# Performance work log

Hardware: AMD Instinct MI355X
Metric: run time of the kernel (lower is better)

Reference implementation:

```python
import jax, jax.numpy as jnp
import numpy as np

# ---- static config (mirrors AttractorCore defaults / chosen shapes) ----
B, N, D, K = 4, 1024, 128, 10          # batch, particles per batch, latent_dim, num_attractors
G = 1e-3                                # gravity_strength
DAMP = 0.95                             # damping
DT = 0.1                                # adaptive_dt initial value (held fixed; adaptive rule not in source)
ITERS = 50                              # num_iterations (fixed; early-exit break removed for jit)
EPS = 1e-6                              # gravitational softening
MAXNORM = 10.0                          # stability constraint: clip position norm
HID = 64                                # PhysicsInformedBoundary hidden_dim


def _mlp2(x, w1, b1, w2, b2):
    # Linear -> Tanh -> Linear  (potential_net / kinetic_net)
    return jnp.tanh(x @ w1 + b1) @ w2 + b2


def setup_inputs() -> dict:
    key = jax.random.key(0)
    ks = jax.random.split(key, 24)

    def lin(k, fan_in, shape):
        return jax.random.normal(k, shape, jnp.float32) / np.sqrt(fan_in)

    x = jax.random.normal(ks[0], (B, N, D), jnp.float32)
    # attractors: random directions normalized to radius 2 (latent_dim != 2 branch)
    ap = jax.random.normal(ks[1], (K, D), jnp.float32)
    ap = ap / jnp.linalg.norm(ap, axis=1, keepdims=True) * 2.0
    am = jnp.ones((K,), jnp.float32) * 0.1
    v0 = jnp.zeros((K, D), jnp.float32)  # registered velocity buffer

    return {
        "x": x,
        "attractor_positions": ap,
        "attractor_masses": am,
        "init_velocities": v0,
        # HamiltonianLayer.potential_net: D -> 2D -> 1
        "pw1": lin(ks[2], D, (D, 2 * D)), "pb1": jnp.zeros((2 * D,), jnp.float32),
        "pw2": lin(ks[3], 2 * D, (2 * D, 1)), "pb2": jnp.zeros((1,), jnp.float32),
        # HamiltonianLayer.kinetic_net: D -> 2D -> 1
        "kw1": lin(ks[4], D, (D, 2 * D)), "kb1": jnp.zeros((2 * D,), jnp.float32),
        "kw2": lin(ks[5], 2 * D, (2 * D, 1)), "kb2": jnp.zeros((1,), jnp.float32),
        # PhysicsInformedBoundary: 2D -> 64 -> 64 -> D
        "bw1": lin(ks[6], 2 * D, (2 * D, HID)), "bb1": jnp.zeros((HID,), jnp.float32),
        "bw2": lin(ks[7], HID, (HID, HID)), "bb2": jnp.zeros((HID,), jnp.float32),
        "bw3": lin(ks[8], HID, (HID, D)), "bb3": jnp.zeros((D,), jnp.float32),
        # field_projection: (3D+4) -> D
        "fw": lin(ks[9], 3 * D + 4, (3 * D + 4, D)), "fb": jnp.zeros((D,), jnp.float32),
    }


def reference(x, attractor_positions, attractor_masses, init_velocities,
              pw1, pb1, pw2, pb2, kw1, kb1, kw2, kb2,
              bw1, bb1, bw2, bb2, bw3, bb3, fw, fb):
    B_, N_, D_ = x.shape
    K_ = attractor_positions.shape[0]

    parts = x.reshape(-1, D_)                                        # [B*N, D]
    masses = jnp.concatenate([jnp.full((B_ * N_,), 0.1, x.dtype),
                              jnp.tile(attractor_masses, B_)])       # [M]
    r0 = jnp.concatenate([parts, jnp.tile(attractor_positions, (B_, 1))], 0)  # [M, D]
    v0 = jnp.concatenate([jnp.zeros_like(parts), jnp.tile(init_velocities, (B_, 1))], 0)
    M = r0.shape[0]
    diag = jnp.eye(M, dtype=bool)

    def pot_sum(p):
        return _mlp2(p, pw1, pb1, pw2, pb2).sum()

    def kin_sum(q):
        return _mlp2(q, kw1, kb1, kw2, kb2).sum()

    @jax.checkpoint
    def step(carry, i):
        r, v = carry
        # all-pairs gravitational acceleration: a_i = G * sum_j m_j (r_j - r_i)/|r_ij|^3
        sq = jnp.sum(r * r, -1)
        d2 = jnp.maximum(sq[:, None] + sq[None, :] - 2.0 * (r @ r.T), EPS)
        inv3 = jnp.where(diag, 0.0, d2 ** -1.5)                      # [M, M]
        w = inv3 * masses[None, :]
        a = G * (w @ r - jnp.sum(w, 1, keepdims=True) * r)
        v = v + a * DT
        r = r + v * DT
        # PINN boundary correction: p + 0.1*tanh(net([p, v]))
        c = jnp.concatenate([r, v], -1)
        h = jnp.tanh(jnp.tanh(c @ bw1 + bb1) @ bw2 + bb2)
        r = r + 0.1 * jnp.tanh(h @ bw3 + bb3)
        # Hamiltonian Euler step every 5 iterations
        do = (i % 5) == 0
        dp = -jax.grad(pot_sum)(r)
        dq = jax.grad(kin_sum)(v)
        r = jnp.where(do, r + 0.01 * dp, r)
        v = jnp.where(do, v + 0.01 * dq, v)
        # damping + stability clip (norm <= MAXNORM)
        v = v * DAMP
        nrm = jnp.linalg.norm(r, axis=-1, keepdims=True)
        r = r * jnp.minimum(1.0, MAXNORM / jnp.maximum(nrm, 1e-12))
        return (r, v), None

    (r, v), _ = jax.lax.scan(step, (r0, v0), jnp.arange(ITERS))

    fp = r[:B_ * N_].reshape(B_, N_, D_)                             # final particles
    fa = r[B_ * N_:].reshape(B_, K_, D_)                             # final attractors

    # ---- compute_attractor_field ----
    pm = jnp.ones((B_, N_), x.dtype)
    am = jnp.broadcast_to(attractor_masses[None, :], (B_, K_))
    allm = jnp.concatenate([pm, am], 1)                              # [B, N+K]
    allp = jnp.concatenate([fp, fa], 1)                              # [B, N+K, D]
    tot = allm.sum(1, keepdims=True)
    com = (allm[..., None] * allp).sum(1) / tot                      # center of mass [B, D]
    centered = allp - com[:, None, :]
    var = (centered ** 2).mean(1)
    skew = (centered ** 3).mean(1)
    # torch.pdist over batch element 0
    p0 = allp[0]
    sq0 = jnp.sum(p0 * p0, -1)
    dmat = jnp.sqrt(jnp.maximum(sq0[:, None] + sq0[None, :] - 2.0 * p0 @ p0.T, 0.0))
    iu, ju = jnp.triu_indices(p0.shape[0], 1)
    dd = dmat[iu, ju]
    stats = jnp.stack([dd.mean(), dd.std(ddof=1), dd.min(), dd.max()])
    stats = jnp.broadcast_to(stats[None, :], (B_, 4))
    feat = jnp.concatenate([com, var, skew, stats], -1)              # [B, 3D+4]
    return feat @ fw + fb                                            # field_projection -> [B, D]


if __name__ == "__main__":
    out = reference(**setup_inputs())
    print(out.shape)
```

## Files before the change

kernel.cpp:

```cpp
#include <hip/hip_runtime.h>
#include <hip/hip_bf16.h>
#include <math.h>

#define DIM    128
#define NPART  4096
#define MREAL  4136
#define MP     4224
#define IB     64
#define NIBR   65
#define JTILE  32
#define NJTR   130
#define NSLICE 8
#define NROW   4136
#define NITER  50
#define NPTS   1034
#define NPAIRS 534061.0
#define WR     16
#define NMLPB  259

typedef __bf16 bf16x8 __attribute__((ext_vector_type(8)));
typedef float  f32x4  __attribute__((ext_vector_type(4)));

__device__ __forceinline__ f32x4 mfma16(bf16x8 a, bf16x8 b, f32x4 c) {
  return __builtin_amdgcn_mfma_f32_16x16x32_bf16(a, b, c, 0, 0, 0);
}
__device__ __forceinline__ float dot4acc(float s, float4 a, float4 b) {
  s = fmaf(a.x, b.x, s); s = fmaf(a.y, b.y, s);
  s = fmaf(a.z, b.z, s); s = fmaf(a.w, b.w, s);
  return s;
}
__device__ __forceinline__ void split3(float x, __bf16& h, __bf16& m, __bf16& l) {
  h = (__bf16)x; float t = x - (float)h;
  m = (__bf16)t; l = (__bf16)(t - (float)m);
}
__device__ __forceinline__ f32x4 mm6(bf16x8 ah, bf16x8 am, bf16x8 al,
                                     bf16x8 bh, bf16x8 bm, bf16x8 bl, f32x4 c) {
  c = mfma16(ah, bh, c);
  c = mfma16(ah, bm, c);
  c = mfma16(am, bh, c);
  c = mfma16(am, bm, c);
  c = mfma16(ah, bl, c);
  c = mfma16(al, bh, c);
  return c;
}
__device__ __forceinline__ f32x4 mm4(bf16x8 ah, bf16x8 am,
                                     bf16x8 bh, bf16x8 bm, f32x4 c) {
  c = mfma16(ah, bh, c);
  c = mfma16(ah, bm, c);
  c = mfma16(am, bh, c);
  c = mfma16(am, bm, c);
  return c;
}
__device__ __forceinline__ int lds_off(int row, int slot) {
  return row * DIM + ((slot ^ ((row >> 2) & 7)) << 2);
}
__device__ __forceinline__ int jmap(int s) {
  return 4 * (s >> 3) + (s & 3) + 16 * ((s >> 2) & 1);
}

__global__ __launch_bounds__(256)
void k_init(const float* __restrict__ x, const float* __restrict__ ap,
            const float* __restrict__ am, const float* __restrict__ v0in,
            float* __restrict__ r, float* __restrict__ v, float* __restrict__ sq)
{
  int wid = threadIdx.x >> 6, ln = threadIdx.x & 63;
  int row = blockIdx.x * 4 + wid;
  int d0 = ln, d1 = ln + 64;
  size_t base = (size_t)row * DIM;
  float r0, r1, w0, w1;
  if (row < NPART) {
    r0 = x[base + d0]; r1 = x[base + d1]; w0 = 0.f; w1 = 0.f;
  } else if (row < MREAL) {
    int k = (row - NPART) % 10;
    r0 = ap[k * DIM + d0]; r1 = ap[k * DIM + d1];
    w0 = v0in[k * DIM + d0]; w1 = v0in[k * DIM + d1];
  } else {
    r0 = r1 = w0 = w1 = 0.f;
  }
  r[base + d0] = r0; r[base + d1] = r1;
  v[base + d0] = w0; v[base + d1] = w1;
  float n2 = r0 * r0 + r1 * r1;
  for (int mk = 1; mk < 64; mk <<= 1) n2 += __shfl_xor(n2, mk);
  if (ln == 0) { sq[row] = n2; }
}

__global__ __launch_bounds__(256)
void k_wprep(const float* __restrict__ bw1, const float* __restrict__ bw2,
             const float* __restrict__ bw3, const float* __restrict__ pw1,
             const float* __restrict__ kw1,
             __bf16* __restrict__ wb1t, __bf16* __restrict__ wb2t,
             __bf16* __restrict__ wb3t, __bf16* __restrict__ wp1t,
             __bf16* __restrict__ wp1r, __bf16* __restrict__ wk1t,
             __bf16* __restrict__ wk1r)
{
  int a = blockIdx.y;
  int e = blockIdx.x * 256 + threadIdx.x;
  float val; __bf16* dst; int size;
  if (a == 0)      { size = 16384; if (e >= size) return; int n = e >> 8, k = e & 255; val = bw1[k * 64 + n];  dst = wb1t; }
  else if (a == 1) { size = 4096;  if (e >= size) return; int n = e >> 6, k = e & 63;  val = bw2[k * 64 + n];  dst = wb2t; }
  else if (a == 2) { size = 8192;  if (e >= size) return; int n = e >> 6, k = e & 63;  val = bw3[k * 128 + n]; dst = wb3t; }
  else if (a == 3) { size = 32768; if (e >= size) return; int n = e >> 7, d = e & 127; val = pw1[d * 256 + n]; dst = wp1t; }
  else if (a == 4) { size = 32768; if (e >= size) return; val = pw1[e]; dst = wp1r; }
  else if (a == 5) { size = 32768; if (e >= size) return; int n = e >> 7, d = e & 127; val = kw1[d * 256 + n]; dst = wk1t; }
  else             { size = 32768; if (e >= size) return; val = kw1[e]; dst = wk1r; }
  __bf16 h, m, l; split3(val, h, m, l);
  dst[e] = h; dst[size + e] = m; dst[2 * size + e] = l;
}

__global__ __launch_bounds__(256)
void k_split(const float* __restrict__ r,
             __bf16* __restrict__ rh, __bf16* __restrict__ rm,
             __bf16* __restrict__ rth, __bf16* __restrict__ rtm, __bf16* __restrict__ rtl)
{
  __shared__ __bf16 hs[32][132], ms2[32][132], ls[32][132];
  const int tid = threadIdx.x;
  const int row = tid >> 3, cg = tid & 7;
  const int grow = blockIdx.x * 32 + row;
  const float* rp = &r[(size_t)grow * DIM + cg * 16];
  float4 f0 = *(const float4*)&rp[0];
  float4 f1 = *(const float4*)&rp[4];
  float4 f2 = *(const float4*)&rp[8];
  float4 f3 = *(const float4*)&rp[12];
  float xs[16] = {f0.x,f0.y,f0.z,f0.w, f1.x,f1.y,f1.z,f1.w,
                  f2.x,f2.y,f2.z,f2.w, f3.x,f3.y,f3.z,f3.w};
  bf16x8 hq[2], mq[2];
  #pragma unroll
  for (int e = 0; e < 16; ++e) {
    float xv = xs[e];
    __bf16 hh, mm, ll; split3(xv, hh, mm, ll);
    hq[e >> 3][e & 7] = hh; mq[e >> 3][e & 7] = mm;
    hs[row][cg * 16 + e] = hh; ms2[row][cg * 16 + e] = mm; ls[row][cg * 16 + e] = ll;
  }
  size_t ob = (size_t)grow * DIM + cg * 16;
  *(bf16x8*)&rh[ob] = hq[0]; *(bf16x8*)&rh[ob + 8] = hq[1];
  *(bf16x8*)&rm[ob] = mq[0]; *(bf16x8*)&rm[ob + 8] = mq[1];
  __syncthreads();
  for (int u = tid; u < 384; u += 256) {
    int s = u >> 7, d = u & 127;
    const __bf16* src = s == 0 ? &hs[0][0] : (s == 1 ? &ms2[0][0] : &ls[0][0]);
    __bf16 col[32];
    #pragma unroll
    for (int j = 0; j < 32; ++j) col[j] = src[j * 132 + d];
    __bf16* dst = (s == 0 ? rth : (s == 1 ? rtm : rtl)) + (size_t)d * MP + blockIdx.x * 32;
    #pragma unroll
    for (int c = 0; c < 4; ++c) {
      bf16x8 q;
      #pragma unroll
      for (int e = 0; e < 8; ++e) q[e] = col[jmap(c * 8 + e)];
      *(bf16x8*)&dst[c * 8] = q;
    }
  }
}

__global__ __launch_bounds__(256, 3)
void k_force(const __bf16* __restrict__ rh, const __bf16* __restrict__ rm,
             const __bf16* __restrict__ rth, const __bf16* __restrict__ rtm,
             const __bf16* __restrict__ rtl,
             const float* __restrict__ sq, const float* __restrict__ am,
             float* __restrict__ apart, float* __restrict__ wsump)
{
  __shared__ __align__(16) __bf16 rjRM[2][JTILE][136];
  __shared__ __align__(16) __bf16 rjT[3][DIM][40];
  __shared__ float sqi_s[IB], sqj_s[JTILE], mj_s[JTILE];

  const int tid = threadIdx.x;
  const int wv = tid >> 6, lane = tid & 63;
  const int lq = lane >> 4, lr = lane & 15;
  const int slice = blockIdx.x;
  const int bi0 = blockIdx.y * IB;

  if (tid < IB) sqi_s[tid] = sq[bi0 + tid];

  const int u1 = tid + 256;
  const int sr0 = tid >> 4, sc0 = tid & 15;
  const int sr1 = u1 >> 4,  sc1 = u1 & 15;
  const int td0 = tid >> 2, te0 = tid & 3;
  const int td1 = u1 >> 2,  te1 = u1 & 3;

  bf16x8 pr[10];
  float psqj = 0.f, pmj = 0.f;

  auto LOADT = [&](int jt) {
    size_t ga0 = (size_t)(jt * JTILE + sr0) * DIM + sc0 * 8;
    size_t ga1 = (size_t)(jt * JTILE + sr1) * DIM + sc1 * 8;
    pr[0] = *(const bf16x8*)&rh[ga0];  pr[1] = *(const bf16x8*)&rm[ga0];
    pr[2] = *(const bf16x8*)&rh[ga1];  pr[3] = *(const bf16x8*)&rm[ga1];
    size_t gb0 = (size_t)td0 * MP + jt * JTILE + te0 * 8;
    size_t gb1 = (size_t)td1 * MP + jt * JTILE + te1 * 8;
    pr[4] = *(const bf16x8*)&rth[gb0]; pr[5] = *(const bf16x8*)&rtm[gb0];
    pr[6] = *(const bf16x8*)&rtl[gb0]; pr[7] = *(const bf16x8*)&rth[gb1];
    pr[8] = *(const bf16x8*)&rtm[gb1]; pr[9] = *(const bf16x8*)&rtl[gb1];
    if (tid < JTILE) {
      int gj = jt * JTILE + tid;
      psqj = sq[gj];
      pmj = gj < NPART ? 0.1f : (gj < MREAL ? am[(gj - NPART) % 10] : 0.f);
    }
  };
  auto STORET = [&]() {
    *(bf16x8*)&rjRM[0][sr0][sc0 * 8] = pr[0];
    *(bf16x8*)&rjRM[1][sr0][sc0 * 8] = pr[1];
    *(bf16x8*)&rjRM[0][sr1][sc1 * 8] = pr[2];
    *(bf16x8*)&rjRM[1][sr1][sc1 * 8] = pr[3];
    *(bf16x8*)&rjT[0][td0][te0 * 8] = pr[4];
    *(bf16x8*)&rjT[1][td0][te0 * 8] = pr[5];
    *(bf16x8*)&rjT[2][td0][te0 * 8] = pr[6];
    *(bf16x8*)&rjT[0][td1][te1 * 8] = pr[7];
    *(bf16x8*)&rjT[1][td1][te1 * 8] = pr[8];
    *(bf16x8*)&rjT[2][td1][te1 * 8] = pr[9];
    if (tid < JTILE) { sqj_s[tid] = psqj; mj_s[tid] = pmj; }
  };

  bf16x8 riH[4], riM[4];
  {
    int gi = bi0 + wv * 16 + lr;
    const __bf16* ph = &rh[(size_t)gi * DIM];
    const __bf16* pm = &rm[(size_t)gi * DIM];
    #pragma unroll
    for (int kc = 0; kc < 4; ++kc) {
      riH[kc] = *(const bf16x8*)&ph[kc * 32 + lq * 8];
      riM[kc] = *(const bf16x8*)&pm[kc * 32 + lq * 8];
    }
  }

  f32x4 accPV[8];
  #pragma unroll
  for (int nt = 0; nt < 8; ++nt) { f32x4 z = {0.f,0.f,0.f,0.f}; accPV[nt] = z; }
  float wsacc = 0.f;

  LOADT(slice);
  STORET();
  __syncthreads();

  for (int jt = slice; jt < NJTR; jt += NSLICE) {
    const int jn = jt + NSLICE;
    const bool more = jn < NJTR;
    if (more) LOADT(jn);

    f32x4 accST[2];
    { f32x4 z = {0.f,0.f,0.f,0.f}; accST[0] = z; accST[1] = z; }
    __builtin_amdgcn_s_setprio(1);
    #pragma unroll
    for (int kc = 0; kc < 4; ++kc) {
      int kq = kc * 4 + lq;
      #pragma unroll
      for (int nt = 0; nt < 2; ++nt) {
        int j = nt * 16 + lr;
        bf16x8 ah = *(const bf16x8*)&rjRM[0][j][kq * 8];
        bf16x8 am = *(const bf16x8*)&rjRM[1][j][kq * 8];
        accST[nt] = mm4(ah, am, riH[kc], riM[kc], accST[nt]);
      }
    }
    __builtin_amdgcn_s_setprio(0);

    bf16x8 aH, aM, aL;
    {
      const int giL = bi0 + wv * 16 + lr;
      const float sqi_l = sqi_s[wv * 16 + lr];
      #pragma unroll
      for (int nt = 0; nt < 2; ++nt)
        #pragma unroll
        for (int rr = 0; rr < 4; ++rr) {
          int jl = nt * 16 + 4 * lq + rr;
          int gj = jt * JTILE + jl;
          float d2 = fmaxf(sqi_l + sqj_s[jl] - 2.f * accST[nt][rr], 1e-6f);
          float rin = rsqrtf(d2);
          float wgt = mj_s[jl] * rin * rin * rin;
          if (giL == gj) wgt = 0.f;
          wsacc += wgt;
          __bf16 wh, wm2, wl2; split3(wgt, wh, wm2, wl2);
          int e = nt * 4 + rr;
          aH[e] = wh; aM[e] = wm2; aL[e] = wl2;
        }
    }

    {
      __builtin_amdgcn_s_setprio(1);
      #pragma unroll
      for (int nt = 0; nt < 8; ++nt) {
        int d = nt * 16 + lr;
        bf16x8 bh = *(const bf16x8*)&rjT[0][d][lq * 8];
        bf16x8 bm = *(const bf16x8*)&rjT[1][d][lq * 8];
        bf16x8 bl = *(const bf16x8*)&rjT[2][d][lq * 8];
        accPV[nt] = mm6(aH, aM, aL, bh, bm, bl, accPV[nt]);
      }
      __builtin_amdgcn_s_setprio(0);
    }

    __syncthreads();
    if (more) STORET();
    __syncthreads();
  }

  {
    float val = wsacc;
    val += __shfl_xor(val, 16);
    val += __shfl_xor(val, 32);
    int gi = bi0 + wv * 16 + lr;
    if (lane < 16 && gi < NROW) wsump[(size_t)slice * NROW + gi] = val;
  }
  #pragma unroll
  for (int nt = 0; nt < 8; ++nt)
    #pragma unroll
    for (int rr = 0; rr < 4; ++rr) {
      int gi = bi0 + wv * 16 + 4 * lq + rr;
      int d = nt * 16 + lr;
      if (gi < NROW) apart[((size_t)slice * NROW + gi) * DIM + d] = accPV[nt][rr];
    }
}

__global__ __launch_bounds__(256)
void k_mlp(float* __restrict__ r, float* __restrict__ v, float* __restrict__ sq,
           const float* __restrict__ apart, const float* __restrict__ wsump,
           const __bf16* __restrict__ wb1t, const __bf16* __restrict__ wb2t,
           const __bf16* __restrict__ wb3t,
           const __bf16* __restrict__ wp1t, const __bf16* __restrict__ wp1r,
           const __bf16* __restrict__ wk1t, const __bf16* __restrict__ wk1r,
           const float* __restrict__ bb1, const float* __restrict__ bb2,
           const float* __restrict__ bb3,
           const float* __restrict__ pb1, const float* __restrict__ pw2,
           const float* __restrict__ kb1, const float* __restrict__ kw2,
           int do_ham)
{
  __shared__ __align__(16) float  Cf[WR][264];
  __shared__ __align__(16) __bf16 Csp[3][WR][264];
  __shared__ __align__(16) __bf16 Hsp[2][3][WR][72];
  __shared__ __align__(16) __bf16 Gsp[3][WR][264];

  const int tid = threadIdx.x;
  const int wv = tid >> 6, lane = tid & 63;
  const int lq = lane >> 4, lr = lane & 15;

  {
    const int row = tid >> 4, c = tid & 15;
    const int grow = blockIdx.x * WR + row;
    const int gsrc = grow < NROW ? grow : 0;
    float s[8] = {0.f,0.f,0.f,0.f,0.f,0.f,0.f,0.f};
    float wsv = 0.f;
    #pragma unroll
    for (int sl = 0; sl < NSLICE; ++sl) {
      const float4* ap4 = (const float4*)&apart[((size_t)sl * NROW + gsrc) * DIM + c * 8];
      float4 t0 = ap4[0], t1 = ap4[1];
      s[0] += t0.x; s[1] += t0.y; s[2] += t0.z; s[3] += t0.w;
      s[4] += t1.x; s[5] += t1.y; s[6] += t1.z; s[7] += t1.w;
      wsv += wsump[(size_t)sl * NROW + gsrc];
    }
    const float4* r4 = (const float4*)&r[(size_t)gsrc * DIM + c * 8];
    const float4* v4 = (const float4*)&v[(size_t)gsrc * DIM + c * 8];
    float4 ra = r4[0], rb = r4[1], va = v4[0], vb = v4[1];
    float re[8] = {ra.x,ra.y,ra.z,ra.w, rb.x,rb.y,rb.z,rb.w};
    float ve[8] = {va.x,va.y,va.z,va.w, vb.x,vb.y,vb.z,vb.w};
    bf16x8 rh8, rm8, rl8, vh8, vm8, vl8;
    #pragma unroll
    for (int e = 0; e < 8; ++e) {
      float a = 1e-3f * (s[e] - wsv * re[e]);
      float vn = ve[e] + 0.1f * a;
      float rn = re[e] + 0.1f * vn;
      Cf[row][c * 8 + e] = rn;
      Cf[row][128 + c * 8 + e] = vn;
      __bf16 h, m, l;
      split3(rn, h, m, l); rh8[e] = h; rm8[e] = m; rl8[e] = l;
      split3(vn, h, m, l); vh8[e] = h; vm8[e] = m; vl8[e] = l;
    }
    *(bf16x8*)&Csp[0][row][c * 8] = rh8; *(bf16x8*)&Csp[0][row][128 + c * 8] = vh8;
    *(bf16x8*)&Csp[1][row][c * 8] = rm8; *(bf16x8*)&Csp[1][row][128 + c * 8] = vm8;
    *(bf16x8*)&Csp[2][row][c * 8] = rl8; *(bf16x8*)&Csp[2][row][128 + c * 8] = vl8;
  }
  __syncthreads();

  {
    f32x4 acc = {0.f, 0.f, 0.f, 0.f};
    const __bf16* b = wb1t + ((size_t)(wv * 16 + lr)) * 256;
    #pragma unroll
    for (int kc = 0; kc < 8; ++kc) {
      int k0 = kc * 32 + lq * 8;
      bf16x8 ah = *(const bf16x8*)&Csp[0][lr][k0];
      bf16x8 am = *(const bf16x8*)&Csp[1][lr][k0];
      bf16x8 al = *(const bf16x8*)&Csp[2][lr][k0];
      bf16x8 b0 = *(const bf16x8*)&b[k0];
      bf16x8 b1 = *(const bf16x8*)&b[16384 + k0];
      bf16x8 b2 = *(const bf16x8*)&b[32768 + k0];
      acc = mm6(ah, am, al, b0, b1, b2, acc);
    }
    int n = wv * 16 + lr;
    float bias = bb1[n];
    #pragma unroll
    for (int reg = 0; reg < 4; ++reg) {
      int i = 4 * lq + reg;
      float h1 = tanhf(acc[reg] + bias);
      __bf16 h, m, l; split3(h1, h, m, l);
      Hsp[0][0][i][n] = h; Hsp[0][1][i][n] = m; Hsp[0][2][i][n] = l;
    }
  }
  __syncthreads();

  {
    f32x4 acc = {0.f, 0.f, 0.f, 0.f};
    const __bf16* b = wb2t + ((size_t)(wv * 16 + lr)) * 64;
    #pragma unroll
    for (int kc = 0; kc < 2; ++kc) {
      int k0 = kc * 32 + lq * 8;
      bf16x8 ah = *(const bf16x8*)&Hsp[0][0][lr][k0];
      bf16x8 am = *(const bf16x8*)&Hsp[0][1][lr][k0];
      bf16x8 al = *(const bf16x8*)&Hsp[0][2][lr][k0];
      bf16x8 b0 = *(const bf16x8*)&b[k0];
      bf16x8 b1 = *(const bf16x8*)&b[4096 + k0];
      bf16x8 b2 = *(const bf16x8*)&b[8192 + k0];
      acc = mm6(ah, am, al, b0, b1, b2, acc);
    }
    int n = wv * 16 + lr;
    float bias = bb2[n];
    #pragma unroll
    for (int reg = 0; reg < 4; ++reg) {
      int i = 4 * lq + reg;
      float h2 = tanhf(acc[reg] + bias);
      __bf16 h, m, l; split3(h2, h, m, l);
      Hsp[1][0][i][n] = h; Hsp[1][1][i][n] = m; Hsp[1][2][i][n] = l;
    }
  }
  __syncthreads();

  {
    f32x4 acc[2];
    { f32x4 z = {0.f,0.f,0.f,0.f}; acc[0] = z; acc[1] = z; }
    #pragma unroll
    for (int kc = 0; kc < 2; ++kc) {
      int k0 = kc * 32 + lq * 8;
      bf16x8 ah = *(const bf16x8*)&Hsp[1][0][lr][k0];
      bf16x8 am = *(const bf16x8*)&Hsp[1][1][lr][k0];
      bf16x8 al = *(const bf16x8*)&Hsp[1][2][lr][k0];
      #pragma unroll
      for (int t = 0; t < 2; ++t) {
        const __bf16* b = wb3t + ((size_t)(t * 64 + wv * 16 + lr)) * 64;
        bf16x8 b0 = *(const bf16x8*)&b[k0];
        bf16x8 b1 = *(const bf16x8*)&b[8192 + k0];
        bf16x8 b2 = *(const bf16x8*)&b[16384 + k0];
        acc[t] = mm6(ah, am, al, b0, b1, b2, acc[t]);
      }
    }
    #pragma unroll
    for (int t = 0; t < 2; ++t) {
      int n = t * 64 + wv * 16 + lr;
      float bias = bb3[n];
      #pragma unroll
      for (int reg = 0; reg < 4; ++reg) {
        int i = 4 * lq + reg;
        float o = tanhf(acc[t][reg] + bias);
        float rn = Cf[i][n] + 0.1f * o;
        Cf[i][n] = rn;
        __bf16 h, m, l; split3(rn, h, m, l);
        Csp[0][i][n] = h; Csp[1][i][n] = m; Csp[2][i][n] = l;
      }
    }
  }
  __syncthreads();

  if (do_ham) {
    {
      f32x4 acc[4];
      #pragma unroll
      for (int t = 0; t < 4; ++t) { f32x4 z = {0.f,0.f,0.f,0.f}; acc[t] = z; }
      #pragma unroll
      for (int kc = 0; kc < 4; ++kc) {
        int k0 = kc * 32 + lq * 8;
        bf16x8 ah = *(const bf16x8*)&Csp[0][lr][k0];
        bf16x8 am = *(const bf16x8*)&Csp[1][lr][k0];
        bf16x8 al = *(const bf16x8*)&Csp[2][lr][k0];
        #pragma unroll
        for (int t = 0; t < 4; ++t) {
          const __bf16* b = wp1t + ((size_t)(t * 64 + wv * 16 + lr)) * 128;
          bf16x8 b0 = *(const bf16x8*)&b[k0];
          bf16x8 b1 = *(const bf16x8*)&b[32768 + k0];
          bf16x8 b2 = *(const bf16x8*)&b[65536 + k0];
          acc[t] = mm6(ah, am, al, b0, b1, b2, acc[t]);
        }
      }
      #pragma unroll
      for (int t = 0; t < 4; ++t) {
        int n = t * 64 + wv * 16 + lr;
        float pb = pb1[n], pws = pw2[n];
        #pragma unroll
        for (int reg = 0; reg < 4; ++reg) {
          int i = 4 * lq + reg;
          float tt = tanhf(acc[t][reg] + pb);
          float g = (1.f - tt * tt) * pws;
          __bf16 h, m, l; split3(g, h, m, l);
          Gsp[0][i][n] = h; Gsp[1][i][n] = m; Gsp[2][i][n] = l;
        }
      }
    }
    __syncthreads();
    {
      f32x4 acc[2];
      { f32x4 z = {0.f,0.f,0.f,0.f}; acc[0] = z; acc[1] = z; }
      #pragma unroll
      for (int kc = 0; kc < 8; ++kc) {
        int k0 = kc * 32 + lq * 8;
        bf16x8 ah = *(const bf16x8*)&Gsp[0][lr][k0];
        bf16x8 am = *(const bf16x8*)&Gsp[1][lr][k0];
        bf16x8 al = *(const bf16x8*)&Gsp[2][lr][k0];
        #pragma unroll
        for (int t = 0; t < 2; ++t) {
          const __bf16* b = wp1r + ((size_t)(t * 64 + wv * 16 + lr)) * 256;
          bf16x8 b0 = *(const bf16x8*)&b[k0];
          bf16x8 b1 = *(const bf16x8*)&b[32768 + k0];
          bf16x8 b2 = *(const bf16x8*)&b[65536 + k0];
          acc[t] = mm6(ah, am, al, b0, b1, b2, acc[t]);
        }
      }
      #pragma unroll
      for (int t = 0; t < 2; ++t)
        #pragma unroll
        for (int reg = 0; reg < 4; ++reg) {
          int i = 4 * lq + reg, d = t * 64 + wv * 16 + lr;
          float rn = Cf[i][d] - 0.01f * acc[t][reg];
          Cf[i][d] = rn;
          __bf16 h, m, l; split3(rn, h, m, l);
          Csp[0][i][d] = h; Csp[1][i][d] = m; Csp[2][i][d] = l;
        }
    }
    __syncthreads();
    {
      f32x4 acc[4];
      #pragma unroll
      for (int t = 0; t < 4; ++t) { f32x4 z = {0.f,0.f,0.f,0.f}; acc[t] = z; }
      #pragma unroll
      for (int kc = 0; kc < 4; ++kc) {
        int k0 = 128 + kc * 32 + lq * 8;
        bf16x8 ah = *(const bf16x8*)&Csp[0][lr][k0];
        bf16x8 am = *(const bf16x8*)&Csp[1][lr][k0];
        bf16x8 al = *(const bf16x8*)&Csp[2][lr][k0];
        #pragma unroll
        for (int t = 0; t < 4; ++t) {
          const __bf16* b = wk1t + ((size_t)(t * 64 + wv * 16 + lr)) * 128;
          int kb = kc * 32 + lq * 8;
          bf16x8 b0 = *(const bf16x8*)&b[kb];
          bf16x8 b1 = *(const bf16x8*)&b[32768 + kb];
          bf16x8 b2 = *(const bf16x8*)&b[65536 + kb];
          acc[t] = mm6(ah, am, al, b0, b1, b2, acc[t]);
        }
      }
      #pragma unroll
      for (int t = 0; t < 4; ++t) {
        int n = t * 64 + wv * 16 + lr;
        float kb = kb1[n], kws = kw2[n];
        #pragma unroll
        for (int reg = 0; reg < 4; ++reg) {
          int i = 4 * lq + reg;
          float tt = tanhf(acc[t][reg] + kb);
          float g = (1.f - tt * tt) * kws;
          __bf16 h, m, l; split3(g, h, m, l);
          Gsp[0][i][n] = h; Gsp[1][i][n] = m; Gsp[2][i][n] = l;
        }
      }
    }
    __syncthreads();
    {
      f32x4 acc[2];
      { f32x4 z = {0.f,0.f,0.f,0.f}; acc[0] = z; acc[1] = z; }
      #pragma unroll
      for (int kc = 0; kc < 8; ++kc) {
        int k0 = kc * 32 + lq * 8;
        bf16x8 ah = *(const bf16x8*)&Gsp[0][lr][k0];
        bf16x8 am = *(const bf16x8*)&Gsp[1][lr][k0];
        bf16x8 al = *(const bf16x8*)&Gsp[2][lr][k0];
        #pragma unroll
        for (int t = 0; t < 2; ++t) {
          const __bf16* b = wk1r + ((size_t)(t * 64 + wv * 16 + lr)) * 256;
          bf16x8 b0 = *(const bf16x8*)&b[k0];
          bf16x8 b1 = *(const bf16x8*)&b[32768 + k0];
          bf16x8 b2 = *(const bf16x8*)&b[65536 + k0];
          acc[t] = mm6(ah, am, al, b0, b1, b2, acc[t]);
        }
      }
      #pragma unroll
      for (int t = 0; t < 2; ++t)
        #pragma unroll
        for (int reg = 0; reg < 4; ++reg) {
          int i = 4 * lq + reg, d = t * 64 + wv * 16 + lr;
          Cf[i][128 + d] += 0.01f * acc[t][reg];
        }
    }
    __syncthreads();
  }

  {
    const int row = tid >> 4, c = tid & 15;
    const int grow = blockIdx.x * WR + row;
    float re[8], ve[8];
    #pragma unroll
    for (int e = 0; e < 8; ++e) {
      re[e] = Cf[row][c * 8 + e];
      ve[e] = Cf[row][128 + c * 8 + e] * 0.95f;
    }
    float n2 = 0.f;
    #pragma unroll
    for (int e = 0; e < 8; ++e) n2 += re[e] * re[e];
    n2 += __shfl_xor(n2, 1); n2 += __shfl_xor(n2, 2);
    n2 += __shfl_xor(n2, 4); n2 += __shfl_xor(n2, 8);
    float nrm = sqrtf(n2);
    float sc = fminf(1.f, 10.f / fmaxf(nrm, 1e-12f));
    if (grow < NROW) {
      float4 o0, o1, w0, w1;
      o0.x = re[0] * sc; o0.y = re[1] * sc; o0.z = re[2] * sc; o0.w = re[3] * sc;
      o1.x = re[4] * sc; o1.y = re[5] * sc; o1.z = re[6] * sc; o1.w = re[7] * sc;
      w0.x = ve[0]; w0.y = ve[1]; w0.z = ve[2]; w0.w = ve[3];
      w1.x = ve[4]; w1.y = ve[5]; w1.z = ve[6]; w1.w = ve[7];
      *(float4*)&r[(size_t)grow * DIM + c * 8] = o0;
      *(float4*)&r[(size_t)grow * DIM + c * 8 + 4] = o1;
      *(float4*)&v[(size_t)grow * DIM + c * 8] = w0;
      *(float4*)&v[(size_t)grow * DIM + c * 8 + 4] = w1;
      if (c == 0) sq[grow] = n2 * sc * sc;
    }
  }
}

__global__ void k_statinit(double* pd_sum, double* pd_sumsq,
                           unsigned* pd_min, unsigned* pd_max)
{
  if (threadIdx.x == 0) {
    *pd_sum = 0.0; *pd_sumsq = 0.0;
    *pd_min = 0x7f7fffffu;
    *pd_max = 0u;
  }
}

__global__ __launch_bounds__(256)
void k_com(const float* __restrict__ r, const float* __restrict__ am,
           float* __restrict__ feat)
{
  int b = blockIdx.x, ch = blockIdx.y;
  int c = threadIdx.x & 31, rg = threadIdx.x >> 5;
  int col = ch * 32 + c;
  __shared__ float red[8][33];
  float amsum = 0.f;
  for (int k = 0; k < 10; ++k) amsum += am[k];
  float tot = 1024.f + amsum;

  float s = 0.f;
  #pragma unroll 4
  for (int p = rg; p < NPTS; p += 8) {
    int row = p < 1024 ? b * 1024 + p : NPART + b * 10 + (p - 1024);
    float m = p < 1024 ? 1.f : am[p - 1024];
    s += m * r[(size_t)row * DIM + col];
  }
  red[rg][c] = s; __syncthreads();
  for (int h = 4; h >= 1; h >>= 1) { if (rg < h) red[rg][c] += red[rg + h][c]; __syncthreads(); }
  float com = red[0][c] / tot;
  __syncthreads();

  float s2 = 0.f, s3 = 0.f;
  #pragma unroll 4
  for (int p = rg; p < NPTS; p += 8) {
    int row = p < 1024 ? b * 1024 + p : NPART + b * 10 + (p - 1024);
    float cc = r[(size_t)row * DIM + col] - com;
    s2 += cc * cc; s3 += cc * cc * cc;
  }
  red[rg][c] = s2; __syncthreads();
  for (int h = 4; h >= 1; h >>= 1) { if (rg < h) red[rg][c] += red[rg + h][c]; __syncthreads(); }
  float var = red[0][c] / 1034.f;
  __syncthreads();
  red[rg][c] = s3; __syncthreads();
  for (int h = 4; h >= 1; h >>= 1) { if (rg < h) red[rg][c] += red[rg + h][c]; __syncthreads(); }
  float skw = red[0][c] / 1034.f;
  if (rg == 0) {
    feat[b * 384 + col]       = com;
    feat[b * 384 + 128 + col] = var;
    feat[b * 384 + 256 + col] = skw;
  }
}

__global__ __launch_bounds__(256)
void k_pdist(const float* __restrict__ r, const float* __restrict__ sq,
             double* pd_sum, double* pd_sumsq, unsigned* pd_min, unsigned* pd_max)
{
  int ta = blockIdx.x, tb = blockIdx.y;
  if (ta > tb) return;
  __shared__ __align__(16) float pa_s[64 * DIM];
  __shared__ __align__(16) float pb_s[64 * DIM];
  __shared__ float sqa_s[64], sqb_s[64];
  const int tid = threadIdx.x;
  const int tx = tid & 15, ty = tid >> 4;

  #pragma unroll
  for (int p = 0; p < 8; ++p) {
    int q = tid + p * 256;
    int row = q >> 5, slot = q & 31;
    int pidx = ta * 64 + row;
    float4 val = make_float4(0.f, 0.f, 0.f, 0.f);
    if (pidx < NPTS) {
      int srow = pidx < 1024 ? pidx : (NPART + pidx - 1024);
      val = *(const float4*)&r[(size_t)srow * DIM + slot * 4];
    }
    *(float4*)&pa_s[lds_off(row, slot)] = val;
    pidx = tb * 64 + row;
    val = make_float4(0.f, 0.f, 0.f, 0.f);
    if (pidx < NPTS) {
      int srow = pidx < 1024 ? pidx : (NPART + pidx - 1024);
      val = *(const float4*)&r[(size_t)srow * DIM + slot * 4];
    }
    *(float4*)&pb_s[lds_off(row, slot)] = val;
  }
  if (tid < 64) {
    int pidx = ta * 64 + tid;
    sqa_s[tid] = pidx < NPTS ? sq[pidx < 1024 ? pidx : NPART + pidx - 1024] : 0.f;
  } else if (tid < 128) {
    int t2 = tid - 64;
    int pidx = tb * 64 + t2;
    sqb_s[t2] = pidx < NPTS ? sq[pidx < 1024 ? pidx : NPART + pidx - 1024] : 0.f;
  }
  __syncthreads();

  const int swi = ty & 7, swj = tx & 7;
  float sv[4][4] = {};
  #pragma unroll 8
  for (int ks = 0; ks < 32; ++ks) {
    int oi = (ks ^ swi) << 2, oj = (ks ^ swj) << 2;
    float4 av[4], bv[4];
    #pragma unroll
    for (int a = 0; a < 4; ++a) av[a] = *(const float4*)&pa_s[(ty * 4 + a) * DIM + oi];
    #pragma unroll
    for (int b = 0; b < 4; ++b) bv[b] = *(const float4*)&pb_s[(tx * 4 + b) * DIM + oj];
    #pragma unroll
    for (int a = 0; a < 4; ++a)
      #pragma unroll
      for (int b = 0; b < 4; ++b) sv[a][b] = dot4acc(sv[a][b], av[a], bv[b]);
  }

  double tsum = 0.0, tsq = 0.0;
  float tmn = 3.402823466e38f, tmx = 0.f;
  #pragma unroll
  for (int a = 0; a < 4; ++a)
    #pragma unroll
    for (int b = 0; b < 4; ++b) {
      int ga = ta * 64 + ty * 4 + a;
      int gb = tb * 64 + tx * 4 + b;
      float d2 = sqa_s[ty * 4 + a] + sqb_s[tx * 4 + b] - 2.f * sv[a][b];
      float dist = sqrtf(fmaxf(d2, 0.f));
      bool ok = (ga < NPTS) && (gb < NPTS) && ((ta != tb) || (ga < gb));
      if (ok) {
        tsum += (double)dist;
        tsq  += (double)dist * (double)dist;
        tmn = fminf(tmn, dist);
        tmx = fmaxf(tmx, dist);
      }
    }
  for (int mk = 1; mk < 64; mk <<= 1) {
    tsum += __shfl_xor(tsum, mk);
    tsq  += __shfl_xor(tsq, mk);
    tmn = fminf(tmn, __shfl_xor(tmn, mk));
    tmx = fmaxf(tmx, __shfl_xor(tmx, mk));
  }
  if ((tid & 63) == 0) {
    atomicAdd(pd_sum, tsum);
    atomicAdd(pd_sumsq, tsq);
    atomicMin(pd_min, __float_as_uint(tmn));
    atomicMax(pd_max, __float_as_uint(tmx));
  }
}

__global__ void k_proj(const float* __restrict__ feat,
                       const double* pd_sum, const double* pd_sumsq,
                       const unsigned* pd_min, const unsigned* pd_max,
                       const float* __restrict__ fw, const float* __restrict__ fb,
                       float* __restrict__ out)
{
  int t = threadIdx.x;
  int b = t >> 7, d = t & 127;
  double sm = *pd_sum, s2 = *pd_sumsq;
  double mean = sm / NPAIRS;
  double var = (s2 - sm * sm / NPAIRS) / (NPAIRS - 1.0);
  float sd = (float)sqrt(var > 0.0 ? var : 0.0);
  float mn = __uint_as_float(*pd_min);
  float mx = __uint_as_float(*pd_max);
  float acc0 = fb[d], acc1 = 0.f, acc2 = 0.f, acc3 = 0.f;
  #pragma unroll 8
  for (int f = 0; f < 384; f += 4) {
    acc0 = fmaf(feat[b * 384 + f + 0], fw[(f + 0) * 128 + d], acc0);
    acc1 = fmaf(feat[b * 384 + f + 1], fw[(f + 1) * 128 + d], acc1);
    acc2 = fmaf(feat[b * 384 + f + 2], fw[(f + 2) * 128 + d], acc2);
    acc3 = fmaf(feat[b * 384 + f + 3], fw[(f + 3) * 128 + d], acc3);
  }
  float acc = (acc0 + acc1) + (acc2 + acc3);
  acc = fmaf((float)mean, fw[384 * 128 + d], acc);
  acc = fmaf(sd,          fw[385 * 128 + d], acc);
  acc = fmaf(mn,          fw[386 * 128 + d], acc);
  acc = fmaf(mx,          fw[387 * 128 + d], acc);
  out[b * 128 + d] = acc;
}

extern "C" void kernel_launch(void* const* d_in, const int* in_sizes, int n_in,
                              void* d_out, int out_size, void* d_ws, size_t ws_size,
                              hipStream_t stream) {
  (void)in_sizes; (void)n_in; (void)out_size; (void)ws_size;
  const float* x   = (const float*)d_in[0];
  const float* ap  = (const float*)d_in[1];
  const float* am  = (const float*)d_in[2];
  const float* v0  = (const float*)d_in[3];
  const float* pw1 = (const float*)d_in[4];
  const float* pb1 = (const float*)d_in[5];
  const float* pw2 = (const float*)d_in[6];
  const float* kw1 = (const float*)d_in[8];
  const float* kb1 = (const float*)d_in[9];
  const float* kw2 = (const float*)d_in[10];
  const float* bw1 = (const float*)d_in[12];
  const float* bb1 = (const float*)d_in[13];
  const float* bw2 = (const float*)d_in[14];
  const float* bb2 = (const float*)d_in[15];
  const float* bw3 = (const float*)d_in[16];
  const float* bb3 = (const float*)d_in[17];
  const float* fw  = (const float*)d_in[18];
  const float* fb  = (const float*)d_in[19];

  char* ws = (char*)d_ws;
  double*   pd_sum   = (double*)(ws + 0);
  double*   pd_sumsq = (double*)(ws + 8);
  unsigned* pd_min   = (unsigned*)(ws + 16);
  unsigned* pd_max   = (unsigned*)(ws + 20);
  float*    feat     = (float*)(ws + 32);
  float*    r        = (float*)(ws + 6176);
  float*    v        = (float*)(ws + 2168864);
  float*    sq       = (float*)(ws + 4331552);
  float*    wsump    = (float*)(ws + 4348448);
  float*    apart    = (float*)(ws + 4480800);
  __bf16*   rh       = (__bf16*)(ws + 21421856);
  __bf16*   rm       = (__bf16*)(ws + 22503200);
  __bf16*   rth      = (__bf16*)(ws + 24665888);
  __bf16*   rtm      = (__bf16*)(ws + 25747232);
  __bf16*   rtl      = (__bf16*)(ws + 26828576);
  __bf16*   wb1t     = (__bf16*)(ws + 27909920);
  __bf16*   wb2t     = (__bf16*)(ws + 28008224);
  __bf16*   wb3t     = (__bf16*)(ws + 28032800);
  __bf16*   wp1t     = (__bf16*)(ws + 28081952);
  __bf16*   wp1r     = (__bf16*)(ws + 28278560);
  __bf16*   wk1t     = (__bf16*)(ws + 28475168);
  __bf16*   wk1r     = (__bf16*)(ws + 28671776);

  k_wprep<<<dim3(128, 7), 256, 0, stream>>>(bw1, bw2, bw3, pw1, kw1,
                                            wb1t, wb2t, wb3t, wp1t, wp1r, wk1t, wk1r);
  k_init<<<MP / 4, 256, 0, stream>>>(x, ap, am, v0, r, v, sq);
  for (int it = 0; it < NITER; ++it) {
    k_split<<<NJTR, 256, 0, stream>>>(r, rh, rm, rth, rtm, rtl);
    k_force<<<dim3(NSLICE, NIBR), 256, 0, stream>>>(rh, rm, rth, rtm, rtl,
                                                    sq, am, apart, wsump);
    k_mlp<<<NMLPB, 256, 0, stream>>>(r, v, sq, apart, wsump,
        wb1t, wb2t, wb3t, wp1t, wp1r, wk1t, wk1r,
        bb1, bb2, bb3, pb1, pw2, kb1, kw2,
        (it % 5) == 0 ? 1 : 0);
  }
  k_statinit<<<1, 64, 0, stream>>>(pd_sum, pd_sumsq, pd_min, pd_max);
  k_com<<<dim3(4, 4), 256, 0, stream>>>(r, am, feat);
  k_pdist<<<dim3(17, 17), 256, 0, stream>>>(r, sq, pd_sum, pd_sumsq, pd_min, pd_max);
  k_proj<<<1, 512, 0, stream>>>(feat, pd_sum, pd_sumsq, pd_min, pd_max, fw, fb,
                                (float*)d_out);
}
```

Measured before the change: 5.267 ms.

## Fuse bf16 split into MLP epilogue and double i-tile per force block

The per-iteration k_split launch is removed. Its work now happens in the k_mlp epilogue, which writes the hi/mid/lo bf16 splits and the transposed tiles straight from shared memory, and k_split runs once before the loop. k_force now handles 128 rows per block (two 16-row m-tiles per wave), so each loaded j-tile feeds twice as many MFMAs. The next-tile prefetch is moved after the weight computation. The trade is more registers and fewer blocks (occupancy hint drops from 3 to 2 blocks per SM, and half as many i-blocks), plus extra shared-memory and global-store work in k_mlp. The transposed-write indexing in k_mlp relies on the jmap permutation pattern, so a mismatch with k_split's layout is a correctness risk.

```diff
diff --git a/kernel.cpp b/kernel.cpp
--- a/kernel.cpp
+++ b/kernel.cpp
@@ -6,8 +6,8 @@
 #define NPART  4096
 #define MREAL  4136
 #define MP     4224
-#define IB     64
-#define NIBR   65
+#define IB     128
+#define NIBT   33
 #define JTILE  32
 #define NJTR   130
 #define NSLICE 8
@@ -19,6 +19,7 @@
 #define NMLPB  259
 
 typedef __bf16 bf16x8 __attribute__((ext_vector_type(8)));
+typedef __bf16 bf16x4 __attribute__((ext_vector_type(4)));
 typedef float  f32x4  __attribute__((ext_vector_type(4)));
 
 __device__ __forceinline__ f32x4 mfma16(bf16x8 a, bf16x8 b, f32x4 c) {
@@ -152,7 +153,7 @@
   }
 }
 
-__global__ __launch_bounds__(256, 3)
+__global__ __launch_bounds__(256, 2)
 void k_force(const __bf16* __restrict__ rh, const __bf16* __restrict__ rm,
              const __bf16* __restrict__ rth, const __bf16* __restrict__ rtm,
              const __bf16* __restrict__ rtl,
@@ -210,22 +211,25 @@
     if (tid < JTILE) { sqj_s[tid] = psqj; mj_s[tid] = pmj; }
   };
 
-  bf16x8 riH[4], riM[4];
-  {
-    int gi = bi0 + wv * 16 + lr;
+  bf16x8 riH[2][4], riM[2][4];
+  #pragma unroll
+  for (int mt = 0; mt < 2; ++mt) {
+    int gi = bi0 + wv * 32 + mt * 16 + lr;
     const __bf16* ph = &rh[(size_t)gi * DIM];
     const __bf16* pm = &rm[(size_t)gi * DIM];
     #pragma unroll
     for (int kc = 0; kc < 4; ++kc) {
-      riH[kc] = *(const bf16x8*)&ph[kc * 32 + lq * 8];
-      riM[kc] = *(const bf16x8*)&pm[kc * 32 + lq * 8];
-    }
-  }
-
-  f32x4 accPV[8];
+      riH[mt][kc] = *(const bf16x8*)&ph[kc * 32 + lq * 8];
+      riM[mt][kc] = *(const bf16x8*)&pm[kc * 32 + lq * 8];
+    }
+  }
+
+  f32x4 accPV[2][8];
   #pragma unroll
-  for (int nt = 0; nt < 8; ++nt) { f32x4 z = {0.f,0.f,0.f,0.f}; accPV[nt] = z; }
-  float wsacc = 0.f;
+  for (int mt = 0; mt < 2; ++mt)
+    #pragma unroll
+    for (int nt = 0; nt < 8; ++nt) { f32x4 z = {0.f,0.f,0.f,0.f}; accPV[mt][nt] = z; }
+  float wsacc[2] = {0.f, 0.f};
 
   LOADT(slice);
   STORET();
@@ -234,10 +238,10 @@
   for (int jt = slice; jt < NJTR; jt += NSLICE) {
     const int jn = jt + NSLICE;
     const bool more = jn < NJTR;
-    if (more) LOADT(jn);
-
-    f32x4 accST[2];
-    { f32x4 z = {0.f,0.f,0.f,0.f}; accST[0] = z; accST[1] = z; }
+
+    f32x4 accST[2][2];
+    { f32x4 z = {0.f,0.f,0.f,0.f};
+      accST[0][0] = z; accST[0][1] = z; accST[1][0] = z; accST[1][1] = z; }
     __builtin_amdgcn_s_setprio(1);
     #pragma unroll
     for (int kc = 0; kc < 4; ++kc) {
@@ -246,32 +250,37 @@
       for (int nt = 0; nt < 2; ++nt) {
         int j = nt * 16 + lr;
         bf16x8 ah = *(const bf16x8*)&rjRM[0][j][kq * 8];
-        bf16x8 am = *(const bf16x8*)&rjRM[1][j][kq * 8];
-        accST[nt] = mm4(ah, am, riH[kc], riM[kc], accST[nt]);
+        bf16x8 am2 = *(const bf16x8*)&rjRM[1][j][kq * 8];
+        accST[0][nt] = mm4(ah, am2, riH[0][kc], riM[0][kc], accST[0][nt]);
+        accST[1][nt] = mm4(ah, am2, riH[1][kc], riM[1][kc], accST[1][nt]);
       }
     }
     __builtin_amdgcn_s_setprio(0);
 
-    bf16x8 aH, aM, aL;
-    {
-      const int giL = bi0 + wv * 16 + lr;
-      const float sqi_l = sqi_s[wv * 16 + lr];
+    bf16x8 aH[2], aM[2], aL[2];
+    #pragma unroll
+    for (int mt = 0; mt < 2; ++mt) {
+      const int il = wv * 32 + mt * 16 + lr;
+      const int giL = bi0 + il;
+      const float sqi_l = sqi_s[il];
       #pragma unroll
       for (int nt = 0; nt < 2; ++nt)
         #pragma unroll
         for (int rr = 0; rr < 4; ++rr) {
           int jl = nt * 16 + 4 * lq + rr;
           int gj = jt * JTILE + jl;
-          float d2 = fmaxf(sqi_l + sqj_s[jl] - 2.f * accST[nt][rr], 1e-6f);
+          float d2 = fmaxf(sqi_l + sqj_s[jl] - 2.f * accST[mt][nt][rr], 1e-6f);
           float rin = rsqrtf(d2);
           float wgt = mj_s[jl] * rin * rin * rin;
           if (giL == gj) wgt = 0.f;
-          wsacc += wgt;
+          wsacc[mt] += wgt;
           __bf16 wh, wm2, wl2; split3(wgt, wh, wm2, wl2);
           int e = nt * 4 + rr;
-          aH[e] = wh; aM[e] = wm2; aL[e] = wl2;
+          aH[mt][e] = wh; aM[mt][e] = wm2; aL[mt][e] = wl2;
         }
     }
+
+    if (more) LOADT(jn);
 
     {
       __builtin_amdgcn_s_setprio(1);
@@ -281,7 +290,8 @@
         bf16x8 bh = *(const bf16x8*)&rjT[0][d][lq * 8];
         bf16x8 bm = *(const bf16x8*)&rjT[1][d][lq * 8];
         bf16x8 bl = *(const bf16x8*)&rjT[2][d][lq * 8];
-        accPV[nt] = mm6(aH, aM, aL, bh, bm, bl, accPV[nt]);
+        accPV[0][nt] = mm6(aH[0], aM[0], aL[0], bh, bm, bl, accPV[0][nt]);
+        accPV[1][nt] = mm6(aH[1], aM[1], aL[1], bh, bm, bl, accPV[1][nt]);
       }
       __builtin_amdgcn_s_setprio(0);
     }
@@ -291,21 +301,24 @@
     __syncthreads();
   }
 
-  {
-    float val = wsacc;
+  #pragma unroll
+  for (int mt = 0; mt < 2; ++mt) {
+    float val = wsacc[mt];
     val += __shfl_xor(val, 16);
     val += __shfl_xor(val, 32);
-    int gi = bi0 + wv * 16 + lr;
+    int gi = bi0 + wv * 32 + mt * 16 + lr;
     if (lane < 16 && gi < NROW) wsump[(size_t)slice * NROW + gi] = val;
   }
   #pragma unroll
-  for (int nt = 0; nt < 8; ++nt)
-    #pragma unroll
-    for (int rr = 0; rr < 4; ++rr) {
-      int gi = bi0 + wv * 16 + 4 * lq + rr;
-      int d = nt * 16 + lr;
-      if (gi < NROW) apart[((size_t)slice * NROW + gi) * DIM + d] = accPV[nt][rr];
-    }
+  for (int mt = 0; mt < 2; ++mt)
+    #pragma unroll
+    for (int nt = 0; nt < 8; ++nt)
+      #pragma unroll
+      for (int rr = 0; rr < 4; ++rr) {
+        int gi = bi0 + wv * 32 + mt * 16 + 4 * lq + rr;
+        int d = nt * 16 + lr;
+        if (gi < NROW) apart[((size_t)slice * NROW + gi) * DIM + d] = accPV[mt][nt][rr];
+      }
 }
 
 __global__ __launch_bounds__(256)
@@ -319,6 +332,9 @@
            const float* __restrict__ bb3,
            const float* __restrict__ pb1, const float* __restrict__ pw2,
            const float* __restrict__ kb1, const float* __restrict__ kw2,
+           __bf16* __restrict__ rh, __bf16* __restrict__ rm,
+           __bf16* __restrict__ rth, __bf16* __restrict__ rtm,
+           __bf16* __restrict__ rtl,
            int do_ham)
 {
   __shared__ __align__(16) float  Cf[WR][264];
@@ -599,17 +615,51 @@
     n2 += __shfl_xor(n2, 4); n2 += __shfl_xor(n2, 8);
     float nrm = sqrtf(n2);
     float sc = fminf(1.f, 10.f / fmaxf(nrm, 1e-12f));
+    float rs[8];
+    #pragma unroll
+    for (int e = 0; e < 8; ++e) rs[e] = re[e] * sc;
+    bf16x8 h8, m8, l8;
+    #pragma unroll
+    for (int e = 0; e < 8; ++e) {
+      __bf16 h, m, l; split3(rs[e], h, m, l);
+      h8[e] = h; m8[e] = m; l8[e] = l;
+    }
+    *(bf16x8*)&Csp[0][row][c * 8] = h8;
+    *(bf16x8*)&Csp[1][row][c * 8] = m8;
+    *(bf16x8*)&Csp[2][row][c * 8] = l8;
     if (grow < NROW) {
       float4 o0, o1, w0, w1;
-      o0.x = re[0] * sc; o0.y = re[1] * sc; o0.z = re[2] * sc; o0.w = re[3] * sc;
-      o1.x = re[4] * sc; o1.y = re[5] * sc; o1.z = re[6] * sc; o1.w = re[7] * sc;
+      o0.x = rs[0]; o0.y = rs[1]; o0.z = rs[2]; o0.w = rs[3];
+      o1.x = rs[4]; o1.y = rs[5]; o1.z = rs[6]; o1.w = rs[7];
       w0.x = ve[0]; w0.y = ve[1]; w0.z = ve[2]; w0.w = ve[3];
       w1.x = ve[4]; w1.y = ve[5]; w1.z = ve[6]; w1.w = ve[7];
       *(float4*)&r[(size_t)grow * DIM + c * 8] = o0;
       *(float4*)&r[(size_t)grow * DIM + c * 8 + 4] = o1;
       *(float4*)&v[(size_t)grow * DIM + c * 8] = w0;
       *(float4*)&v[(size_t)grow * DIM + c * 8 + 4] = w1;
+      *(bf16x8*)&rh[(size_t)grow * DIM + c * 8] = h8;
+      *(bf16x8*)&rm[(size_t)grow * DIM + c * 8] = m8;
       if (c == 0) sq[grow] = n2 * sc * sc;
+    }
+  }
+  __syncthreads();
+  {
+    const int grow0 = blockIdx.x * WR;
+    const int b32 = grow0 >> 5;
+    const int half = blockIdx.x & 1;
+    for (int u = tid; u < 384; u += 256) {
+      int s = u >> 7, d = u & 127;
+      __bf16* dst = (s == 0 ? rth : (s == 1 ? rtm : rtl))
+                    + (size_t)d * MP + b32 * 32 + half * 4;
+      #pragma unroll
+      for (int a = 0; a < 4; ++a) {
+        if (grow0 + 4 * a + 4 <= NROW) {
+          bf16x4 q;
+          #pragma unroll
+          for (int c2 = 0; c2 < 4; ++c2) q[c2] = Csp[s][4 * a + c2][d];
+          *(bf16x4*)&dst[a * 8] = q;
+        }
+      }
     }
   }
 }
@@ -838,13 +888,14 @@
   k_wprep<<<dim3(128, 7), 256, 0, stream>>>(bw1, bw2, bw3, pw1, kw1,
                                             wb1t, wb2t, wb3t, wp1t, wp1r, wk1t, wk1r);
   k_init<<<MP / 4, 256, 0, stream>>>(x, ap, am, v0, r, v, sq);
+  k_split<<<MP / 32, 256, 0, stream>>>(r, rh, rm, rth, rtm, rtl);
   for (int it = 0; it < NITER; ++it) {
-    k_split<<<NJTR, 256, 0, stream>>>(r, rh, rm, rth, rtm, rtl);
-    k_force<<<dim3(NSLICE, NIBR), 256, 0, stream>>>(rh, rm, rth, rtm, rtl,
+    k_force<<<dim3(NSLICE, NIBT), 256, 0, stream>>>(rh, rm, rth, rtm, rtl,
                                                     sq, am, apart, wsump);
     k_mlp<<<NMLPB, 256, 0, stream>>>(r, v, sq, apart, wsump,
         wb1t, wb2t, wb3t, wp1t, wp1r, wk1t, wk1r,
         bb1, bb2, bb3, pb1, pw2, kb1, kw2,
+        rh, rm, rth, rtm, rtl,
         (it % 5) == 0 ? 1 : 0);
   }
   k_statinit<<<1, 64, 0, stream>>>(pd_sum, pd_sumsq, pd_min, pd_max);
```

Measured after the change: 5.455 ms. +3.6%, slower.
